# Optimization experiments

Measured on AMD Instinct MI355X. Metric: run time of the kernel, lower is better.

The kernel has to match this reference:

```python
import jax, jax.numpy as jnp
import numpy as np
import math

QUERY_DIM = 1024
KEY_DIM = 768
VALUE_DIM = 768
NUM_HEADS = 16
HEAD_DIM = QUERY_DIM // NUM_HEADS


def setup_inputs() -> dict:
    key = jax.random.key(0)
    ks = jax.random.split(key, 11)
    B, Sq, Skv = 4, 2048, 2048
    query = jax.random.normal(ks[0], (B, Sq, QUERY_DIM), dtype=jnp.float32)
    k_in = jax.random.normal(ks[1], (B, Skv, KEY_DIM), dtype=jnp.float32)
    v_in = jax.random.normal(ks[2], (B, Skv, VALUE_DIM), dtype=jnp.float32)
    # Linear weights stored as [in, out] (y = x @ W + b), equivalent to torch's x @ W^T.
    def lin(k, fan_in, fan_out):
        bound = 1.0 / math.sqrt(fan_in)
        kw, kb = jax.random.split(k)
        W = jax.random.uniform(kw, (fan_in, fan_out), minval=-bound, maxval=bound, dtype=jnp.float32)
        b = jax.random.uniform(kb, (fan_out,), minval=-bound, maxval=bound, dtype=jnp.float32)
        return W, b
    Wq, bq = lin(ks[3], QUERY_DIM, QUERY_DIM)
    Wk, bk = lin(ks[4], KEY_DIM, QUERY_DIM)
    Wv, bv = lin(ks[5], VALUE_DIM, QUERY_DIM)
    Wo, bo = lin(ks[6], QUERY_DIM, QUERY_DIM)
    return {"query": query, "key": k_in, "value": v_in,
            "Wq": Wq, "bq": bq, "Wk": Wk, "bk": bk,
            "Wv": Wv, "bv": bv, "Wo": Wo, "bo": bo}


def reference(query, key, value, Wq, bq, Wk, bk, Wv, bv, Wo, bo):
    B, Sq, _ = query.shape
    H, D = NUM_HEADS, HEAD_DIM
    # Projections -> [B, H, S, D]
    Q = (query @ Wq + bq).reshape(B, Sq, H, D).transpose(0, 2, 1, 3)
    K = (key @ Wk + bk).reshape(B, -1, H, D).transpose(0, 2, 1, 3)
    V = (value @ Wv + bv).reshape(B, -1, H, D).transpose(0, 2, 1, 3)
    scale = 1.0 / math.sqrt(D)
    scores = jnp.einsum('bhqd,bhkd->bhqk', Q, K) * scale  # [B,H,Sq,Skv]
    weights = jax.nn.softmax(scores, axis=-1)
    attended = jnp.einsum('bhqk,bhkd->bhqd', weights, V)
    attended = attended.transpose(0, 2, 1, 3).reshape(B, Sq, H * D)
    # torch .squeeze(1): no-op since Sq > 1
    return attended @ Wo + bo
```

## Files before the change

### kernel.cpp

```cpp
#include <hip/hip_runtime.h>

#define B_ 4
#define SQ 2048
#define SKV 2048
#define DMODEL 1024
#define DKV 768
#define NH 16
#define DH 64

typedef unsigned short u16;
typedef __bf16 bf16x4 __attribute__((ext_vector_type(4)));
typedef __bf16 bf16x8 __attribute__((ext_vector_type(8)));
typedef float f32x4 __attribute__((ext_vector_type(4)));
typedef float f32x16 __attribute__((ext_vector_type(16)));

__device__ __forceinline__ u16 f2bf(float f) {
  union { __bf16 b; u16 u; } cv;
  cv.b = (__bf16)f;
  return cv.u;
}

__device__ __forceinline__ unsigned cvtpk(float lo, float hi) {
  unsigned r;
  asm("v_cvt_pk_bf16_f32 %0, %1, %2" : "=v"(r) : "v"(lo), "v"(hi));
  return r;
}

__device__ __forceinline__ float fexp2(float x) {
  float r;
  asm("v_exp_f32 %0, %1" : "=v"(r) : "v"(x));
  return r;
}

#define GLDS(gp, lp) __builtin_amdgcn_global_load_lds(                         \
    (const __attribute__((address_space(1))) unsigned*)(gp),                   \
    (__attribute__((address_space(3))) unsigned*)(lp), 16, 0, 0)


__global__ __launch_bounds__(256)
void wt4_kernel(const float* __restrict__ W0, const float* __restrict__ W1,
                const float* __restrict__ W2, const float* __restrict__ W3,
                u16* __restrict__ T0, u16* __restrict__ T1,
                u16* __restrict__ T2, u16* __restrict__ T3) {
  const int z = blockIdx.z;
  const float* W = (z == 0) ? W0 : (z == 1) ? W1 : (z == 2) ? W2 : W3;
  u16* T = (z == 0) ? T0 : (z == 1) ? T1 : (z == 2) ? T2 : T3;
  const int K = (z == 1 || z == 2) ? DKV : DMODEL;
  const int N = DMODEL;
  int n0 = blockIdx.x * 32, k0 = blockIdx.y * 32;
  if (k0 >= K) return;
  __shared__ float tl[32][33];
  int tx = threadIdx.x, ty = threadIdx.y;
#pragma unroll
  for (int p = 0; p < 4; ++p)
    tl[ty + 8 * p][tx] = W[(size_t)(k0 + ty + 8 * p) * N + n0 + tx];
  __syncthreads();
#pragma unroll
  for (int p = 0; p < 4; ++p) {
    int n = n0 + ty + 8 * p;
    int kx = (k0 + tx) ^ ((n & 7) << 3);
    T[(size_t)n * K + kx] = f2bf(tl[tx][ty + 8 * p]);
  }
}

__global__ __launch_bounds__(256)
void qkv_kernel(const float* __restrict__ Aq, const float* __restrict__ Ak,
                const float* __restrict__ Av,
                const u16* __restrict__ Wtq, const u16* __restrict__ Wtk,
                const u16* __restrict__ Wtv,
                const float* __restrict__ bq, const float* __restrict__ bk,
                const float* __restrict__ bv,
                float sclq,
                u16* __restrict__ Qp, u16* __restrict__ Kp, u16* __restrict__ Vt) {
  __shared__ __align__(16) u16 Alds[128][88];
  __shared__ __align__(16) u16 Blds[128][64];
  const int z = blockIdx.z;
  const float* Af = (z == 0) ? Aq : (z == 1) ? Ak : Av;
  const u16* Wt = (z == 0) ? Wtq : (z == 1) ? Wtk : Wtv;
  const float* bias = (z == 0) ? bq : (z == 1) ? bk : bv;
  const int K = (z == 0) ? DMODEL : DKV;
  const float oscale = (z == 0) ? sclq : 1.0f;

  const int t = threadIdx.x;
  const int l = t & 63;
  const int lx = l & 15, lg = l >> 4;
  const int wid = t >> 6;
  const int wr = wid >> 1, wc = wid & 1;

  int flat = blockIdx.y * 8 + blockIdx.x;
  int by = (flat & 7) * 8 + ((flat >> 3) & 7);
  int bx = flat >> 6;
  const int m0 = by * 128, n0 = bx * 128;

  const int srow = l >> 3;
  const int scol = (l & 7) * 8;
  const int bswz = (lx & 7) << 3;

  f32x4 acc[4][4];
#pragma unroll
  for (int i = 0; i < 4; ++i)
#pragma unroll
    for (int j = 0; j < 4; ++j) acc[i][j] = (f32x4){0.f, 0.f, 0.f, 0.f};

  const int arow = t >> 4;
  const int acol = (t & 15) * 4;
  const float* abase = Af + (size_t)(m0 + arow) * K + acol;

  float4 areg[8];
#pragma unroll
  for (int p = 0; p < 8; ++p)
    areg[p] = *(const float4*)(abase + (size_t)p * 16 * K);

  for (int k0 = 0; k0 < K; k0 += 64) {
    __syncthreads();
#pragma unroll
    for (int j = 0; j < 4; ++j) {
      int row = wid * 32 + j * 8;
      GLDS(Wt + (size_t)(n0 + row + srow) * K + k0 + scol, &Blds[row][0]);
    }
#pragma unroll
    for (int p = 0; p < 8; ++p) {
      union { bf16x4 v; uint2 u; } cv;
      cv.v[0] = (__bf16)areg[p].x; cv.v[1] = (__bf16)areg[p].y;
      cv.v[2] = (__bf16)areg[p].z; cv.v[3] = (__bf16)areg[p].w;
      *(uint2*)(&Alds[p * 16 + arow][acol]) = cv.u;
    }
    __syncthreads();
    if ((k0 + 64) < K) {
#pragma unroll
      for (int p = 0; p < 8; ++p)
        areg[p] = *(const float4*)(abase + (size_t)p * 16 * K + k0 + 64);
    }
#pragma unroll
    for (int kk = 0; kk < 64; kk += 32) {
      bf16x8 af[4], bfr[4];
#pragma unroll
      for (int i = 0; i < 4; ++i)
        af[i] = *(const bf16x8*)(&Alds[wr * 64 + i * 16 + lx][kk + lg * 8]);
#pragma unroll
      for (int j = 0; j < 4; ++j)
        bfr[j] = *(const bf16x8*)(&Blds[wc * 64 + j * 16 + lx][(kk + lg * 8) ^ bswz]);
#pragma unroll
      for (int i = 0; i < 4; ++i)
#pragma unroll
        for (int j = 0; j < 4; ++j)
          acc[i][j] = __builtin_amdgcn_mfma_f32_16x16x32_bf16(af[i], bfr[j], acc[i][j], 0, 0, 0);
    }
  }
#pragma unroll
  for (int j = 0; j < 4; ++j) {
    int col = n0 + wc * 64 + j * 16 + lx;
    float bv = bias[col];
#pragma unroll
    for (int i = 0; i < 4; ++i) {
      int rowb = m0 + wr * 64 + i * 16 + lg * 4;
      f32x4 c = acc[i][j];
      if (z == 2) {
        int b = rowb >> 11, s = rowb & 2047;
        int h = col >> 6, d = col & 63;
        u16* vt = Vt + (size_t)((b * NH + h) * DH + d) * SKV + s;
        union { bf16x4 v; uint2 u; } cv;
        cv.v[0] = (__bf16)(c[0] + bv); cv.v[1] = (__bf16)(c[1] + bv);
        cv.v[2] = (__bf16)(c[2] + bv); cv.v[3] = (__bf16)(c[3] + bv);
        *(uint2*)vt = cv.u;
      } else {
        u16* op = (z == 0) ? Qp : Kp;
#pragma unroll
        for (int r = 0; r < 4; ++r)
          op[(size_t)(rowb + r) * DMODEL + col] = f2bf((c[r] + bv) * oscale);
      }
    }
  }
}

__global__ __launch_bounds__(256)
void oproj_kernel(const u16* __restrict__ Ab, const u16* __restrict__ Wt,
                  const float* __restrict__ bias, float* __restrict__ out_) {
  const int N = DMODEL, K = DMODEL;
  __shared__ __align__(16) u16 Alds[128][64];
  __shared__ __align__(16) u16 Blds[128][64];
  const int t = threadIdx.x;
  const int l = t & 63;
  const int lx = l & 15, lg = l >> 4;
  const int wid = t >> 6;
  const int wr = wid >> 1, wc = wid & 1;

  int flat = blockIdx.y * 8 + blockIdx.x;
  int by = (flat & 7) * 8 + ((flat >> 3) & 7);
  int bx = flat >> 6;
  const int m0 = by * 128, n0 = bx * 128;

  const int srow = l >> 3;
  const int scol = (l & 7) * 8;
  const int swz = (lx & 7) << 3;

  f32x4 acc[4][4];
#pragma unroll
  for (int i = 0; i < 4; ++i)
#pragma unroll
    for (int j = 0; j < 4; ++j) acc[i][j] = (f32x4){0.f, 0.f, 0.f, 0.f};

  for (int k0 = 0; k0 < K; k0 += 64) {
    __syncthreads();
#pragma unroll
    for (int j = 0; j < 4; ++j) {
      int row = wid * 32 + j * 8;
      GLDS(Wt + (size_t)(n0 + row + srow) * K + k0 + scol, &Blds[row][0]);
      GLDS(Ab + (size_t)(m0 + row + srow) * K + k0 + scol, &Alds[row][0]);
    }
    __syncthreads();
#pragma unroll
    for (int kk = 0; kk < 64; kk += 32) {
      bf16x8 af[4], bfr[4];
#pragma unroll
      for (int i = 0; i < 4; ++i)
        af[i] = *(const bf16x8*)(&Alds[wr * 64 + i * 16 + lx][(kk + lg * 8) ^ swz]);
#pragma unroll
      for (int j = 0; j < 4; ++j)
        bfr[j] = *(const bf16x8*)(&Blds[wc * 64 + j * 16 + lx][(kk + lg * 8) ^ swz]);
#pragma unroll
      for (int i = 0; i < 4; ++i)
#pragma unroll
        for (int j = 0; j < 4; ++j)
          acc[i][j] = __builtin_amdgcn_mfma_f32_16x16x32_bf16(af[i], bfr[j], acc[i][j], 0, 0, 0);
    }
  }
#pragma unroll
  for (int j = 0; j < 4; ++j) {
    int col = n0 + wc * 64 + j * 16 + lx;
    float bv = bias[col];
#pragma unroll
    for (int i = 0; i < 4; ++i) {
      int rowb = m0 + wr * 64 + i * 16 + lg * 4;
      f32x4 c = acc[i][j];
#pragma unroll
      for (int r = 0; r < 4; ++r)
        out_[(size_t)(rowb + r) * N + col] = c[r] + bv;
    }
  }
}

#define KVB 64
#define KP 72

__global__ __launch_bounds__(512)
void attn_kernel(const u16* __restrict__ Qp, const u16* __restrict__ Kp,
                 const u16* __restrict__ Vt, u16* __restrict__ Att) {
  __shared__ __align__(16) u16 Klds[2][KVB][KP];
  __shared__ __align__(16) u16 Vlds[2][DH][KP];
  const int t = threadIdx.x;
  const int l = t & 63;
  const int ql = l & 31, hi = l >> 5;
  const int wid = t >> 6;

  const int flat = blockIdx.y * 8 + blockIdx.x;
  const int xcd = flat & 7;
  const int rest = flat >> 3;
  const int bh = xcd * 8 + (rest & 7);
  const int qb = rest >> 3;
  const int b = bh >> 4, h = bh & 15;
  const int q = qb * 256 + wid * 32 + ql;

  bf16x8 qf[4];
  const u16* qbase = Qp + (size_t)(b * SQ + q) * DMODEL + h * 64 + hi * 8;
#pragma unroll
  for (int ds = 0; ds < 4; ++ds) qf[ds] = *(const bf16x8*)(qbase + ds * 16);

  bf16x8 ones;
  {
    union { unsigned u[4]; bf16x8 v; } o;
    o.u[0] = o.u[1] = o.u[2] = o.u[3] = 0x3F803F80u;
    ones = o.v;
  }
  f32x16 z16;
#pragma unroll
  for (int r = 0; r < 16; ++r) z16[r] = 0.f;

  f32x16 acc0, acc1, sacc;
#pragma unroll
  for (int r = 0; r < 16; ++r) { acc0[r] = 0.f; acc1[r] = 0.f; sacc[r] = 0.f; }

  const int sr = t >> 3;
  const int sc = (t & 7) * 8;
  const u16* kg = Kp + (size_t)(b * SKV) * DMODEL + h * 64;
  const u16* vg = Vt + ((size_t)(b * NH + h) * DH + sr) * SKV;

  {
    uint4 k0 = *(const uint4*)(kg + (size_t)sr * DMODEL + sc);
    uint4 v0 = *(const uint4*)(vg + sc);
    *(uint4*)(&Klds[0][sr][sc]) = k0;
    *(uint4*)(&Vlds[0][sr][sc]) = v0;
  }
  int cur = 0;

  for (int kv0 = 0; kv0 < SKV; kv0 += KVB) {
    uint4 kr0, vr0;
    const bool pf = (kv0 + KVB) < SKV;
    if (pf) {
      kr0 = *(const uint4*)(kg + (size_t)(kv0 + KVB + sr) * DMODEL + sc);
      vr0 = *(const uint4*)(vg + kv0 + KVB + sc);
    }
    __syncthreads();

    f32x16 st0, st1;
    __builtin_amdgcn_s_setprio(1);
    {
      bf16x8 k0 = *(const bf16x8*)(&Klds[cur][ql][hi * 8]);
      bf16x8 k1 = *(const bf16x8*)(&Klds[cur][32 + ql][hi * 8]);
      st0 = __builtin_amdgcn_mfma_f32_32x32x16_bf16(k0, qf[0], z16, 0, 0, 0);
      st1 = __builtin_amdgcn_mfma_f32_32x32x16_bf16(k1, qf[0], z16, 0, 0, 0);
    }
#pragma unroll
    for (int ds = 1; ds < 4; ++ds) {
      bf16x8 k0 = *(const bf16x8*)(&Klds[cur][ql][ds * 16 + hi * 8]);
      bf16x8 k1 = *(const bf16x8*)(&Klds[cur][32 + ql][ds * 16 + hi * 8]);
      st0 = __builtin_amdgcn_mfma_f32_32x32x16_bf16(k0, qf[ds], st0, 0, 0, 0);
      st1 = __builtin_amdgcn_mfma_f32_32x32x16_bf16(k1, qf[ds], st1, 0, 0, 0);
    }
    __builtin_amdgcn_s_setprio(0);

#pragma unroll
    for (int r = 0; r < 16; ++r) { st0[r] = fexp2(st0[r]); st1[r] = fexp2(st1[r]); }

    __builtin_amdgcn_s_setprio(1);
#pragma unroll
    for (int tt = 0; tt < 2; ++tt) {
      const f32x16& stt = tt ? st1 : st0;
      unsigned pk[8];
#pragma unroll
      for (int j = 0; j < 8; ++j) pk[j] = cvtpk(stt[2 * j], stt[2 * j + 1]);
#pragma unroll
      for (int ksl = 0; ksl < 2; ++ksl) {
        auto wA = __builtin_amdgcn_permlane32_swap(pk[4 * ksl + 0], pk[4 * ksl + 2], false, false);
        auto wB = __builtin_amdgcn_permlane32_swap(pk[4 * ksl + 1], pk[4 * ksl + 3], false, false);
        union { unsigned w[4]; bf16x8 v; } pfr;
        pfr.w[0] = (unsigned)wA[0]; pfr.w[1] = (unsigned)wB[0];
        pfr.w[2] = (unsigned)wA[1]; pfr.w[3] = (unsigned)wB[1];
        int ks = tt * 2 + ksl;
        bf16x8 v0 = *(const bf16x8*)(&Vlds[cur][ql][ks * 16 + hi * 8]);
        bf16x8 v1 = *(const bf16x8*)(&Vlds[cur][32 + ql][ks * 16 + hi * 8]);
        acc0 = __builtin_amdgcn_mfma_f32_32x32x16_bf16(v0, pfr.v, acc0, 0, 0, 0);
        acc1 = __builtin_amdgcn_mfma_f32_32x32x16_bf16(v1, pfr.v, acc1, 0, 0, 0);
        sacc = __builtin_amdgcn_mfma_f32_32x32x16_bf16(ones, pfr.v, sacc, 0, 0, 0);
      }
    }
    __builtin_amdgcn_s_setprio(0);

    if (pf) {
      int nxt = cur ^ 1;
      *(uint4*)(&Klds[nxt][sr][sc]) = kr0;
      *(uint4*)(&Vlds[nxt][sr][sc]) = vr0;
    }
    cur ^= 1;
  }

  float inv = 1.0f / sacc[0];
  u16* ob = Att + (size_t)(b * SQ + q) * DMODEL + h * 64;
  const int oswz = (ql & 7) << 3;
#pragma unroll
  for (int dt = 0; dt < 2; ++dt) {
    const f32x16& a = dt ? acc1 : acc0;
#pragma unroll
    for (int g = 0; g < 4; ++g) {
      unsigned w0 = cvtpk(a[4 * g] * inv, a[4 * g + 1] * inv);
      unsigned w1 = cvtpk(a[4 * g + 2] * inv, a[4 * g + 3] * inv);
      *(uint2*)(ob + ((dt * 32 + g * 8 + hi * 4) ^ oswz)) = make_uint2(w0, w1);
    }
  }
}

extern "C" void kernel_launch(void* const* d_in, const int* in_sizes, int n_in,
                              void* d_out, int out_size, void* d_ws, size_t ws_size,
                              hipStream_t stream) {
  const float* query = (const float*)d_in[0];
  const float* key   = (const float*)d_in[1];
  const float* value = (const float*)d_in[2];
  const float* Wq = (const float*)d_in[3];
  const float* bq = (const float*)d_in[4];
  const float* Wk = (const float*)d_in[5];
  const float* bk = (const float*)d_in[6];
  const float* Wv = (const float*)d_in[7];
  const float* bv = (const float*)d_in[8];
  const float* Wo = (const float*)d_in[9];
  const float* bo = (const float*)d_in[10];
  float* out = (float*)d_out;

  u16* ws = (u16*)d_ws;
  const size_t MTOK = (size_t)B_ * SQ;
  u16* Qp  = ws;
  u16* Kp  = Qp + MTOK * DMODEL;
  u16* Vtb = Kp + MTOK * DMODEL;
  u16* Att = Vtb + MTOK * DMODEL;
  u16* WqT = Att + MTOK * DMODEL;
  u16* WkT = WqT + (size_t)DMODEL * DMODEL;
  u16* WvT = WkT + (size_t)DKV * DMODEL;
  u16* WoT = WvT + (size_t)DKV * DMODEL;

  const float SCL = 0.18033688011112042f;

  dim3 tb(32, 8);
  wt4_kernel<<<dim3(DMODEL / 32, DMODEL / 32, 4), tb, 0, stream>>>(
      Wq, Wk, Wv, Wo, WqT, WkT, WvT, WoT);

  qkv_kernel<<<dim3(DMODEL / 128, MTOK / 128, 3), 256, 0, stream>>>(
      query, key, value, WqT, WkT, WvT, bq, bk, bv, SCL, Qp, Kp, Vtb);

  attn_kernel<<<dim3(SQ / 256, B_ * NH), 512, 0, stream>>>(Qp, Kp, Vtb, Att);

  oproj_kernel<<<dim3(DMODEL / 128, MTOK / 128), 256, 0, stream>>>(Att, WoT, bo, out);
}
```

Baseline: 178.7 us.

## Pre-cast QKV activations to swizzled bf16 and load them via global_load_lds

Adds a separate cast kernel that converts the fp32 query/key/value activations to bf16 with an XOR-swizzled column layout. The QKV GEMM then streams A tiles straight into LDS with global_load_lds, as it already does for the weights, instead of loading fp32 into registers, converting and storing to LDS. This removes register pressure and per-iteration conversion work from the GEMM inner loop. In exchange it adds an extra kernel launch plus a full fp32 read and bf16 write/read round trip of the activations through global memory, and it drops the register prefetch of the next A tile.

New measurement: 187.0 us. 1.05x slower.

```diff
diff --git a/kernel.cpp b/kernel.cpp
--- a/kernel.cpp
+++ b/kernel.cpp
@@ -36,6 +36,26 @@
     (const __attribute__((address_space(1))) unsigned*)(gp),                   \
     (__attribute__((address_space(3))) unsigned*)(lp), 16, 0, 0)
 
+
+__global__ __launch_bounds__(256)
+void cast3_kernel(const float* __restrict__ Aq, const float* __restrict__ Ak,
+                  const float* __restrict__ Av,
+                  u16* __restrict__ Qb, u16* __restrict__ Kb, u16* __restrict__ Vb) {
+  const int z = blockIdx.y;
+  const float* src = (z == 0) ? Aq : (z == 1) ? Ak : Av;
+  u16* dst = (z == 0) ? Qb : (z == 1) ? Kb : Vb;
+  const int K = (z == 0) ? DMODEL : DKV;
+  const int row = blockIdx.x;
+  const int t = threadIdx.x;
+  const int c4 = t * 4;
+  if (c4 >= K) return;
+  float4 v = *(const float4*)(src + (size_t)row * K + c4);
+  union { bf16x4 b; uint2 u; } cv;
+  cv.b[0] = (__bf16)v.x; cv.b[1] = (__bf16)v.y;
+  cv.b[2] = (__bf16)v.z; cv.b[3] = (__bf16)v.w;
+  int kx = c4 ^ ((row & 7) << 3);
+  *(uint2*)(dst + (size_t)row * K + kx) = cv.u;
+}
 
 __global__ __launch_bounds__(256)
 void wt4_kernel(const float* __restrict__ W0, const float* __restrict__ W1,
@@ -64,18 +84,18 @@
 }
 
 __global__ __launch_bounds__(256)
-void qkv_kernel(const float* __restrict__ Aq, const float* __restrict__ Ak,
-                const float* __restrict__ Av,
+void qkv_kernel(const u16* __restrict__ Qbf, const u16* __restrict__ Kbf,
+                const u16* __restrict__ Vbf,
                 const u16* __restrict__ Wtq, const u16* __restrict__ Wtk,
                 const u16* __restrict__ Wtv,
                 const float* __restrict__ bq, const float* __restrict__ bk,
                 const float* __restrict__ bv,
                 float sclq,
                 u16* __restrict__ Qp, u16* __restrict__ Kp, u16* __restrict__ Vt) {
-  __shared__ __align__(16) u16 Alds[128][88];
+  __shared__ __align__(16) u16 Alds[128][64];
   __shared__ __align__(16) u16 Blds[128][64];
   const int z = blockIdx.z;
-  const float* Af = (z == 0) ? Aq : (z == 1) ? Ak : Av;
+  const u16* Ab = (z == 0) ? Qbf : (z == 1) ? Kbf : Vbf;
   const u16* Wt = (z == 0) ? Wtq : (z == 1) ? Wtk : Wtv;
   const float* bias = (z == 0) ? bq : (z == 1) ? bk : bv;
   const int K = (z == 0) ? DMODEL : DKV;
@@ -94,22 +114,13 @@
 
   const int srow = l >> 3;
   const int scol = (l & 7) * 8;
-  const int bswz = (lx & 7) << 3;
+  const int swz = (lx & 7) << 3;
 
   f32x4 acc[4][4];
 #pragma unroll
   for (int i = 0; i < 4; ++i)
 #pragma unroll
     for (int j = 0; j < 4; ++j) acc[i][j] = (f32x4){0.f, 0.f, 0.f, 0.f};
-
-  const int arow = t >> 4;
-  const int acol = (t & 15) * 4;
-  const float* abase = Af + (size_t)(m0 + arow) * K + acol;
-
-  float4 areg[8];
-#pragma unroll
-  for (int p = 0; p < 8; ++p)
-    areg[p] = *(const float4*)(abase + (size_t)p * 16 * K);
 
   for (int k0 = 0; k0 < K; k0 += 64) {
     __syncthreads();
@@ -117,29 +128,18 @@
     for (int j = 0; j < 4; ++j) {
       int row = wid * 32 + j * 8;
       GLDS(Wt + (size_t)(n0 + row + srow) * K + k0 + scol, &Blds[row][0]);
-    }
-#pragma unroll
-    for (int p = 0; p < 8; ++p) {
-      union { bf16x4 v; uint2 u; } cv;
-      cv.v[0] = (__bf16)areg[p].x; cv.v[1] = (__bf16)areg[p].y;
-      cv.v[2] = (__bf16)areg[p].z; cv.v[3] = (__bf16)areg[p].w;
-      *(uint2*)(&Alds[p * 16 + arow][acol]) = cv.u;
+      GLDS(Ab + (size_t)(m0 + row + srow) * K + k0 + scol, &Alds[row][0]);
     }
     __syncthreads();
-    if ((k0 + 64) < K) {
-#pragma unroll
-      for (int p = 0; p < 8; ++p)
-        areg[p] = *(const float4*)(abase + (size_t)p * 16 * K + k0 + 64);
-    }
 #pragma unroll
     for (int kk = 0; kk < 64; kk += 32) {
       bf16x8 af[4], bfr[4];
 #pragma unroll
       for (int i = 0; i < 4; ++i)
-        af[i] = *(const bf16x8*)(&Alds[wr * 64 + i * 16 + lx][kk + lg * 8]);
+        af[i] = *(const bf16x8*)(&Alds[wr * 64 + i * 16 + lx][(kk + lg * 8) ^ swz]);
 #pragma unroll
       for (int j = 0; j < 4; ++j)
-        bfr[j] = *(const bf16x8*)(&Blds[wc * 64 + j * 16 + lx][(kk + lg * 8) ^ bswz]);
+        bfr[j] = *(const bf16x8*)(&Blds[wc * 64 + j * 16 + lx][(kk + lg * 8) ^ swz]);
 #pragma unroll
       for (int i = 0; i < 4; ++i)
 #pragma unroll
@@ -395,15 +395,20 @@
   u16* WkT = WqT + (size_t)DMODEL * DMODEL;
   u16* WvT = WkT + (size_t)DKV * DMODEL;
   u16* WoT = WvT + (size_t)DKV * DMODEL;
+  u16* Qbf = Att;
+  u16* Kbf = WoT + (size_t)DMODEL * DMODEL;
+  u16* Vbf = Kbf + MTOK * DKV;
 
   const float SCL = 0.18033688011112042f;
+
+  cast3_kernel<<<dim3(MTOK, 3), 256, 0, stream>>>(query, key, value, Qbf, Kbf, Vbf);
 
   dim3 tb(32, 8);
   wt4_kernel<<<dim3(DMODEL / 32, DMODEL / 32, 4), tb, 0, stream>>>(
       Wq, Wk, Wv, Wo, WqT, WkT, WvT, WoT);
 
   qkv_kernel<<<dim3(DMODEL / 128, MTOK / 128, 3), 256, 0, stream>>>(
-      query, key, value, WqT, WkT, WvT, bq, bk, bv, SCL, Qp, Kp, Vtb);
+      Qbf, Kbf, Vbf, WqT, WkT, WvT, bq, bk, bv, SCL, Qp, Kp, Vtb);
 
   attn_kernel<<<dim3(SQ / 256, B_ * NH), 512, 0, stream>>>(Qp, Kp, Vtb, Att);
 
```
